# Performance work log

Measured on AMD Instinct MI355X. Metric: run time of the kernel, lower is better.

## Reference

```python
import jax, jax.numpy as jnp
import numpy as np
from jax import lax

NUM_CNNS = 300
INPUT_LEN = 608
NUM_CLASSES = 50
FILTER = 19
POOL = 7
HIDDEN = 100
BATCH = 256
L_CONV = INPUT_LEN - FILTER + 1          # 590
L_POOL = (L_CONV - POOL) // POOL + 1     # 84
EPS = 1e-5


def setup_inputs() -> dict:
    key = jax.random.key(0)
    ks = jax.random.split(key, 24)
    U, H = NUM_CNNS, HIDDEN
    d = {}
    d["x"] = jax.random.normal(ks[0], (BATCH, 4, INPUT_LEN), dtype=jnp.float32)
    # conv1: grouped Conv1d(4*U -> U, k=19, groups=U) on replicated input == dense Conv1d(4 -> U)
    d["w1"] = jax.random.normal(ks[1], (U, 4, FILTER), dtype=jnp.float32) * 0.1
    d["b1"] = jax.random.normal(ks[2], (U,), dtype=jnp.float32) * 0.05
    d["g1"] = jax.random.uniform(ks[3], (U,), dtype=jnp.float32, minval=0.5, maxval=1.5)
    d["be1"] = jax.random.normal(ks[4], (U,), dtype=jnp.float32) * 0.05
    d["m1"] = jax.random.normal(ks[5], (U,), dtype=jnp.float32) * 0.05
    d["v1"] = jax.random.uniform(ks[6], (U,), dtype=jnp.float32, minval=0.5, maxval=1.5)
    # grouped 1x1 conv: per-unit Linear 84 -> 100
    d["w2"] = jax.random.normal(ks[7], (U, H, L_POOL), dtype=jnp.float32) * (1.0 / np.sqrt(L_POOL))
    d["b2"] = jax.random.normal(ks[8], (U, H), dtype=jnp.float32) * 0.05
    d["g2"] = jax.random.uniform(ks[9], (U, H), dtype=jnp.float32, minval=0.5, maxval=1.5)
    d["be2"] = jax.random.normal(ks[10], (U, H), dtype=jnp.float32) * 0.05
    d["m2"] = jax.random.normal(ks[11], (U, H), dtype=jnp.float32) * 0.05
    d["v2"] = jax.random.uniform(ks[12], (U, H), dtype=jnp.float32, minval=0.5, maxval=1.5)
    # grouped 1x1 conv: per-unit Linear 100 -> 1
    d["w3"] = jax.random.normal(ks[13], (U, H), dtype=jnp.float32) * (1.0 / np.sqrt(H))
    d["b3"] = jax.random.normal(ks[14], (U,), dtype=jnp.float32) * 0.05
    d["g3"] = jax.random.uniform(ks[15], (U,), dtype=jnp.float32, minval=0.5, maxval=1.5)
    d["be3"] = jax.random.normal(ks[16], (U,), dtype=jnp.float32) * 0.05
    d["m3"] = jax.random.normal(ks[17], (U,), dtype=jnp.float32) * 0.05
    d["v3"] = jax.random.uniform(ks[18], (U,), dtype=jnp.float32, minval=0.5, maxval=1.5)
    # final Linear(U -> num_classes)
    d["wf"] = jax.random.normal(ks[19], (NUM_CLASSES, U), dtype=jnp.float32) * (1.0 / np.sqrt(U))
    d["bf"] = jax.random.normal(ks[20], (NUM_CLASSES,), dtype=jnp.float32) * 0.05
    return d


def _bn(y, g, be, m, v):
    return (y - m) * (g * lax.rsqrt(v + EPS)) + be


def reference(x, w1, b1, g1, be1, m1, v1, w2, b2, g2, be2, m2, v2,
              w3, b3, g3, be3, m3, v3, wf, bf):
    # conv1 (replicate + grouped conv == dense conv over 4 channels)
    y = lax.conv_general_dilated(x, w1, window_strides=(1,), padding='VALID',
                                 dimension_numbers=('NCH', 'OIH', 'NCH'))  # [B,U,590]
    y = y + b1[None, :, None]
    y = _bn(y, g1[None, :, None], be1[None, :, None], m1[None, :, None], v1[None, :, None])
    y = jnp.exp(y)  # ExpActivation
    # MaxPool1d(7,7): 590 -> 84 (uses first 588 positions)
    B = y.shape[0]
    y = y[:, :, :L_POOL * POOL].reshape(B, NUM_CNNS, L_POOL, POOL).max(axis=-1)  # [B,U,84]
    # per-unit MLP 84 -> 100 (grouped 1x1 conv) + BN + ReLU (dropout is eval-mode identity)
    h = jnp.einsum('buf,uof->buo', y, w2) + b2[None]  # [B,U,100]
    h = _bn(h, g2[None], be2[None], m2[None], v2[None])
    h = jax.nn.relu(h)
    # per-unit 100 -> 1 + BN + ReLU
    z = jnp.einsum('buo,uo->bu', h, w3) + b3[None]  # [B,U]
    z = _bn(z, g3[None], be3[None], m3[None], v3[None])
    z = jax.nn.relu(z)
    # final Linear
    return z @ wf.T + bf
```

## Files before the change

kernel.cpp:

```cpp
#include <hip/hip_runtime.h>
#include <hip/hip_bf16.h>

#define BATCH    256
#define NU       300
#define LIN      608
#define FILT     19
#define LPOOL    84
#define POOL     7
#define HID      100
#define NCLS     50
#define EPS      1e-5f
#define KP       96
#define NP       112
#define LDK      104
#define WROW     104
#define WBROWS   320
#define TCHUNK   112
#define MTN      19
#define BH       128
#define CSTR     116

typedef __attribute__((ext_vector_type(8))) short short8;
typedef __attribute__((ext_vector_type(4))) float float4v;
typedef __attribute__((ext_vector_type(4))) unsigned short us4;

#define LDS_WAIT() __asm__ __volatile__("s_waitcnt lgkmcnt(0)" ::: "memory")

__device__ __forceinline__ unsigned short f2bf(float f) {
    unsigned u = __float_as_uint(f);
    u += 0x7fffu + ((u >> 16) & 1u);
    return (unsigned short)(u >> 16);
}
__device__ __forceinline__ float bf2f(unsigned short h) {
    return __uint_as_float(((unsigned)h) << 16);
}

__global__ void k_prep(const float* __restrict__ w1, const float* __restrict__ x,
                       const float* __restrict__ b1, const float* __restrict__ g1,
                       const float* __restrict__ be1, const float* __restrict__ m1,
                       const float* __restrict__ v1,
                       unsigned short* __restrict__ Wbh,
                       unsigned short* __restrict__ Wbl,
                       unsigned int* __restrict__ xc,
                       float2* __restrict__ s1c1)
{
    const int idx = blockIdx.x * 256 + threadIdx.x;
    const int NW = WBROWS * WROW;
    if (idx < NW) {
        const int u = idx / WROW, kk = idx - u * WROW;
        float wv = 0.f;
        if (u < NU && kk < 96) {
            const int c = kk / 24, tap = kk - 24 * c;
            if (tap < FILT) wv = w1[(u * 4 + c) * FILT + tap];
        }
        const unsigned short hi = f2bf(wv);
        Wbh[idx] = hi;
        Wbl[idx] = f2bf(wv - bf2f(hi));
    }
    const int j = idx - NW;
    if (j >= 0 && j < BATCH * 4 * LIN) {
        const float xv = x[j];
        const unsigned short hi = f2bf(xv);
        const unsigned short lo = f2bf(xv - bf2f(hi));
        xc[j] = (unsigned)hi | ((unsigned)lo << 16);
    }
    const int j2 = j - BATCH * 4 * LIN;
    if (j2 >= 0 && j2 < MTN * 16) {
        float2 v = {0.f, 0.f};
        if (j2 < NU) {
            const float s = g1[j2] * rsqrtf(v1[j2] + EPS);
            v.x = s;
            v.y = (b1[j2] - m1[j2]) * s + be1[j2];
        }
        s1c1[j2] = v;
    }
}

__global__ __launch_bounds__(256, 3)
void k_conv7d(const unsigned short* __restrict__ Wbh,
              const unsigned short* __restrict__ Wbl,
              const unsigned int* __restrict__ xc,
              const float2* __restrict__ s1c1,
              unsigned short* __restrict__ ypool)
{
    __shared__ __align__(16) unsigned short Bh[TCHUNK * LDK];
    __shared__ __align__(16) float Cs[4][16 * CSTR];

    const int tid = threadIdx.x;
    const int b   = blockIdx.x;
    const int tc  = blockIdx.y;
    const int t0  = TCHUNK * tc;
    const int NT  = (tc == 5) ? 2 : 7;

    for (int i = tid; i < TCHUNK * 12; i += 256) {
        const int trow = i / 12;
        if (trow >= 16 * NT) continue;
        const int rem   = i - 12 * trow;
        const int c     = rem / 3;
        const int third = rem - 3 * c;
        const int kkb   = 24 * c + 8 * third;
        const int tt0   = t0 + trow + 8 * third;
        const unsigned int* src = xc + ((b * 4 + c) * LIN + tt0);

        unsigned int w[8];
        if (third < 2 && tt0 + 8 <= LIN) {
            const uint4 v0 = *(const uint4*)(src);
            const uint4 v1 = *(const uint4*)(src + 4);
            w[0] = v0.x; w[1] = v0.y; w[2] = v0.z; w[3] = v0.w;
            w[4] = v1.x; w[5] = v1.y; w[6] = v1.z; w[7] = v1.w;
        } else {
#pragma unroll
            for (int j = 0; j < 8; ++j) {
                const int tap = 8 * third + j;
                const int tt  = tt0 + j;
                unsigned int v = 0;
                if (tap < FILT && tt < LIN) v = src[j];
                w[j] = v;
            }
        }
        short8 hv;
#pragma unroll
        for (int j = 0; j < 8; ++j) hv[j] = (short)(w[j] & 0xffffu);
        *(short8*)(&Bh[trow * LDK + kkb]) = hv;
    }
    __syncthreads();

    const int lane = tid & 63;
    const int n    = lane & 15;
    const int quad = lane >> 4;
    const int wave = tid >> 6;
    float* Csw = Cs[wave];

    const int u_l = lane & 15;
    const int wq  = lane >> 4;
    const int pg0 = 16 * tc + 4 * wq;

    const int jend = 5 * wave + ((wave == 3) ? 4 : 5);
    for (int mt0 = 5 * wave; mt0 < jend; mt0 += 2) {
        const bool two = (mt0 + 1 < jend);

        short8 a0h[3], a0l[3], a1h[3], a1l[3];
        {
            const unsigned short* wrh = Wbh + (size_t)(mt0 * 16 + n) * WROW;
            const unsigned short* wrl = Wbl + (size_t)(mt0 * 16 + n) * WROW;
#pragma unroll
            for (int s = 0; s < 3; ++s) {
                a0h[s] = *(const short8*)(wrh + 32 * s + 8 * quad);
                a0l[s] = *(const short8*)(wrl + 32 * s + 8 * quad);
            }
            const int m1r = two ? (mt0 + 1) : mt0;
            const unsigned short* wrh1 = Wbh + (size_t)(m1r * 16 + n) * WROW;
            const unsigned short* wrl1 = Wbl + (size_t)(m1r * 16 + n) * WROW;
#pragma unroll
            for (int s = 0; s < 3; ++s) {
                a1h[s] = *(const short8*)(wrh1 + 32 * s + 8 * quad);
                a1l[s] = *(const short8*)(wrl1 + 32 * s + 8 * quad);
            }
        }

        float4v acc[2][7];
#pragma unroll
        for (int t2 = 0; t2 < 2; ++t2)
#pragma unroll
            for (int nt = 0; nt < 7; ++nt)
                acc[t2][nt] = (float4v){0.f, 0.f, 0.f, 0.f};

#pragma unroll
        for (int nt = 0; nt < 7; ++nt) {
            if (nt < NT) {
                short8 bhf[3];
#pragma unroll
                for (int s = 0; s < 3; ++s)
                    bhf[s] = *(const short8*)(&Bh[(16 * nt + n) * LDK + 32 * s + 8 * quad]);
#pragma unroll
                for (int s = 0; s < 3; ++s)
                    acc[0][nt] = __builtin_amdgcn_mfma_f32_16x16x32_bf16(
                        bhf[s], a0h[s], acc[0][nt], 0, 0, 0);
#pragma unroll
                for (int s = 0; s < 3; ++s)
                    acc[0][nt] = __builtin_amdgcn_mfma_f32_16x16x32_bf16(
                        bhf[s], a0l[s], acc[0][nt], 0, 0, 0);
                if (two) {
#pragma unroll
                    for (int s = 0; s < 3; ++s)
                        acc[1][nt] = __builtin_amdgcn_mfma_f32_16x16x32_bf16(
                            bhf[s], a1h[s], acc[1][nt], 0, 0, 0);
#pragma unroll
                    for (int s = 0; s < 3; ++s)
                        acc[1][nt] = __builtin_amdgcn_mfma_f32_16x16x32_bf16(
                            bhf[s], a1l[s], acc[1][nt], 0, 0, 0);
                }
            }
        }

#pragma unroll
        for (int t2 = 0; t2 < 2; ++t2) {
            if (t2 == 1 && !two) break;
            const int mt = mt0 + t2;

            LDS_WAIT();
#pragma unroll
            for (int nt = 0; nt < 7; ++nt) {
                if (nt < NT)
                    *(float4v*)(&Csw[n * CSTR + 16 * nt + 4 * quad]) = acc[t2][nt];
            }
            LDS_WAIT();

            float rv[28];
#pragma unroll
            for (int r7 = 0; r7 < 7; ++r7)
                *(float4v*)(&rv[4 * r7]) =
                    *(const float4v*)(&Csw[u_l * CSTR + 28 * wq + 4 * r7]);

            const int uglob = mt * 16 + u_l;
            const float2 sc = s1c1[uglob];
            us4 pk;
#pragma unroll
            for (int w4 = 0; w4 < 4; ++w4) {
                const int pg = pg0 + w4;
                unsigned short ov = 0;
                if (pg < LPOOL) {
                    float m0 = fmaxf(rv[7 * w4 + 0], rv[7 * w4 + 1]);
                    float m1 = fmaxf(rv[7 * w4 + 2], rv[7 * w4 + 3]);
                    float m2 = fmaxf(rv[7 * w4 + 4], rv[7 * w4 + 5]);
                    m0 = fmaxf(m0, rv[7 * w4 + 6]);
                    ov = f2bf(__expf(fmaf(fmaxf(fmaxf(m0, m1), m2), sc.x, sc.y)));
                }
                pk[w4] = ov;
            }
            if (uglob < NU)
                *(us4*)(&ypool[((size_t)b * NU + uglob) * KP + pg0]) = pk;
        }
    }
}

__global__ __launch_bounds__(256, 3)
void k_mlp(const unsigned short* __restrict__ ypool,
           const float* __restrict__ w2, const float* __restrict__ b2,
           const float* __restrict__ g2, const float* __restrict__ be2,
           const float* __restrict__ m2, const float* __restrict__ v2,
           const float* __restrict__ w3, const float* __restrict__ b3,
           const float* __restrict__ g3, const float* __restrict__ be3,
           const float* __restrict__ m3, const float* __restrict__ v3,
           float* __restrict__ zbuf)
{
    __shared__ __align__(16) unsigned short As[NP * LDK];
    __shared__ __align__(16) unsigned short Bs[BH * LDK];
    __shared__ __align__(16) float4 cs4[NP];

    const int tid = threadIdx.x;
    const int u   = blockIdx.x;
    const int b0  = blockIdx.y * BH;

    {
        const float* src = w2 + (size_t)u * HID * LPOOL;
        for (int c = tid; c < HID * (LPOOL / 4); c += 256) {
            const int o  = c / (LPOOL / 4);
            const int kc = (c % (LPOOL / 4)) * 4;
            const float4 v = *(const float4*)(src + o * LPOOL + kc);
            unsigned short* d = &As[o * LDK + kc];
            d[0] = f2bf(v.x); d[1] = f2bf(v.y); d[2] = f2bf(v.z); d[3] = f2bf(v.w);
        }
        for (int c = tid; c < HID * 6; c += 256) {
            const int o = c / 6, kc = LPOOL + (c % 6) * 2;
            *(unsigned*)(&As[o * LDK + kc]) = 0;
        }
        for (int c = tid; c < (NP - HID) * (KP / 2); c += 256) {
            const int o = HID + c / (KP / 2), kc = (c % (KP / 2)) * 2;
            *(unsigned*)(&As[o * LDK + kc]) = 0;
        }
    }
    {
        const unsigned short* ys = ypool + (size_t)u * KP;
        for (int c = tid; c < BH * (KP / 8); c += 256) {
            const int n  = c / (KP / 8);
            const int kc = (c % (KP / 8)) * 8;
            *(short8*)(&Bs[n * LDK + kc]) =
                *(const short8*)(ys + (size_t)(b0 + n) * NU * KP + kc);
        }
    }
    if (tid < NP) {
        float4 cv = {0.f, 0.f, 0.f, 0.f};
        if (tid < HID) {
            const int uo = u * HID + tid;
            const float s = g2[uo] * rsqrtf(v2[uo] + EPS);
            cv.x = s;
            cv.y = (b2[uo] - m2[uo]) * s + be2[uo];
            cv.z = w3[uo];
        }
        cs4[tid] = cv;
    }
    __syncthreads();

    const int lane = tid & 63;
    const int wave = tid >> 6;
    const int col  = lane & 15;
    const int quad = lane >> 4;

    short8 bf_[2][3];
#pragma unroll
    for (int j = 0; j < 2; ++j) {
        const int brow = 16 * (2 * wave + j) + col;
#pragma unroll
        for (int s = 0; s < 3; ++s)
            bf_[j][s] = *(const short8*)(&Bs[brow * LDK + 32 * s + 8 * quad]);
    }

    float zp0 = 0.f, zp1 = 0.f;
#pragma unroll
    for (int mt = 0; mt < 7; ++mt) {
        short8 af[3];
#pragma unroll
        for (int s = 0; s < 3; ++s)
            af[s] = *(const short8*)(&As[(16 * mt + col) * LDK + 32 * s + 8 * quad]);

        float4v a0 = {0.f, 0.f, 0.f, 0.f}, a1 = {0.f, 0.f, 0.f, 0.f};
#pragma unroll
        for (int s = 0; s < 3; ++s) {
            a0 = __builtin_amdgcn_mfma_f32_16x16x32_bf16(af[s], bf_[0][s], a0, 0, 0, 0);
            a1 = __builtin_amdgcn_mfma_f32_16x16x32_bf16(af[s], bf_[1][s], a1, 0, 0, 0);
        }
#pragma unroll
        for (int r = 0; r < 4; ++r) {
            const float4 cv = cs4[16 * mt + 4 * quad + r];
            zp0 = fmaf(fmaxf(fmaf(a0[r], cv.x, cv.y), 0.f), cv.z, zp0);
            zp1 = fmaf(fmaxf(fmaf(a1[r], cv.x, cv.y), 0.f), cv.z, zp1);
        }
    }

    zp0 += __shfl_xor(zp0, 16); zp0 += __shfl_xor(zp0, 32);
    zp1 += __shfl_xor(zp1, 16); zp1 += __shfl_xor(zp1, 32);

    if (quad == 0) {
        const float s3 = g3[u] * rsqrtf(v3[u] + EPS);
        const float c3 = (b3[u] - m3[u]) * s3 + be3[u];
        const int bA = b0 + 16 * (2 * wave + 0) + col;
        const int bB = b0 + 16 * (2 * wave + 1) + col;
        zbuf[(size_t)u * BATCH + bA] = fmaxf(fmaf(zp0, s3, c3), 0.f);
        zbuf[(size_t)u * BATCH + bB] = fmaxf(fmaf(zp1, s3, c3), 0.f);
    }
}

__global__ __launch_bounds__(256, 4)
void k_final(const float* __restrict__ zbuf, const float* __restrict__ wf,
             const float* __restrict__ bf, float* __restrict__ out)
{
    __shared__ float red[4][64];
    const int nc   = blockIdx.x;
    const int bq   = blockIdx.y;
    const int lane = threadIdx.x & 63;
    const int wave = threadIdx.x >> 6;
    const int b    = bq * 64 + lane;

    float a0 = 0.f, a1 = 0.f, a2 = 0.f;
    const int u0 = wave * 75;
#pragma unroll 5
    for (int i = 0; i < 75; i += 3) {
        a0 = fmaf(zbuf[(size_t)(u0 + i + 0) * BATCH + b], wf[nc * NU + u0 + i + 0], a0);
        a1 = fmaf(zbuf[(size_t)(u0 + i + 1) * BATCH + b], wf[nc * NU + u0 + i + 1], a1);
        a2 = fmaf(zbuf[(size_t)(u0 + i + 2) * BATCH + b], wf[nc * NU + u0 + i + 2], a2);
    }
    red[wave][lane] = (a0 + a1) + a2;
    __syncthreads();
    if (threadIdx.x < 64) {
        const float s = (red[0][lane] + red[1][lane]) + (red[2][lane] + red[3][lane]);
        out[(size_t)b * NCLS + nc] = s + bf[nc];
    }
}

extern "C" void kernel_launch(void* const* d_in, const int* in_sizes, int n_in,
                              void* d_out, int out_size, void* d_ws, size_t ws_size,
                              hipStream_t stream)
{
    const float* x   = (const float*)d_in[0];
    const float* w1  = (const float*)d_in[1];
    const float* b1  = (const float*)d_in[2];
    const float* g1  = (const float*)d_in[3];
    const float* be1 = (const float*)d_in[4];
    const float* m1  = (const float*)d_in[5];
    const float* v1  = (const float*)d_in[6];
    const float* w2  = (const float*)d_in[7];
    const float* b2  = (const float*)d_in[8];
    const float* g2  = (const float*)d_in[9];
    const float* be2 = (const float*)d_in[10];
    const float* m2  = (const float*)d_in[11];
    const float* v2  = (const float*)d_in[12];
    const float* w3  = (const float*)d_in[13];
    const float* b3  = (const float*)d_in[14];
    const float* g3  = (const float*)d_in[15];
    const float* be3 = (const float*)d_in[16];
    const float* m3  = (const float*)d_in[17];
    const float* v3  = (const float*)d_in[18];
    const float* wf  = (const float*)d_in[19];
    const float* bf  = (const float*)d_in[20];

    unsigned short* ypool = (unsigned short*)d_ws;
    float* zbuf = (float*)((char*)d_ws + 14745600);
    unsigned short* Wbh = (unsigned short*)((char*)d_ws + 15052800);
    unsigned short* Wbl = (unsigned short*)((char*)d_ws + 15119360);
    unsigned int*   xc  = (unsigned int*)((char*)d_ws + 15185920);
    float2*         sc1 = (float2*)((char*)d_ws + 17676288);

    const int prep_elems = WBROWS * WROW + BATCH * 4 * LIN + MTN * 16;
    k_prep<<<(prep_elems + 255) / 256, 256, 0, stream>>>(
        w1, x, b1, g1, be1, m1, v1, Wbh, Wbl, xc, sc1);

    dim3 gc(BATCH, 6);
    k_conv7d<<<gc, 256, 0, stream>>>(Wbh, Wbl, xc, sc1, ypool);

    dim3 gm(NU, BATCH / BH);
    k_mlp<<<gm, 256, 0, stream>>>(ypool, w2, b2, g2, be2, m2, v2,
                                  w3, b3, g3, be3, m3, v3, zbuf);

    dim3 gf(NCLS, 4);
    k_final<<<gf, 256, 0, stream>>>(zbuf, wf, bf, (float*)d_out);
}
```

Measured before the change: 149.1 us.

## Precompute padded bf16 w2 in prep and drop LDS staging in MLP kernel

The fp32-to-bf16 conversion and padding of the per-unit w2 weights moves out of k_mlp into the prep kernel, which writes a padded bf16 copy laid out for MFMA fragment loads. k_mlp no longer stages weights or activations in shared memory. Each wave loads its A and B fragments straight from global memory. The batch tile shrinks from 128 to 64, doubling the grid, and the occupancy hint rises to 4 blocks per SM. This removes the LDS fill, its barrier cost and the repeated fp32 conversion. In exchange it adds a prep pass over all of w2, scattered global fragment reads, and more re-reads of the weight copy across batch tiles.

```diff
diff --git a/kernel.cpp b/kernel.cpp
--- a/kernel.cpp
+++ b/kernel.cpp
@@ -17,7 +17,6 @@
 #define WBROWS   320
 #define TCHUNK   112
 #define MTN      19
-#define BH       128
 #define CSTR     116
 
 typedef __attribute__((ext_vector_type(8))) short short8;
@@ -38,11 +37,12 @@
 __global__ void k_prep(const float* __restrict__ w1, const float* __restrict__ x,
                        const float* __restrict__ b1, const float* __restrict__ g1,
                        const float* __restrict__ be1, const float* __restrict__ m1,
-                       const float* __restrict__ v1,
+                       const float* __restrict__ v1, const float* __restrict__ w2,
                        unsigned short* __restrict__ Wbh,
                        unsigned short* __restrict__ Wbl,
                        unsigned int* __restrict__ xc,
-                       float2* __restrict__ s1c1)
+                       float2* __restrict__ s1c1,
+                       unsigned short* __restrict__ w2c)
 {
     const int idx = blockIdx.x * 256 + threadIdx.x;
     const int NW = WBROWS * WROW;
@@ -73,6 +73,16 @@
             v.y = (b1[j2] - m1[j2]) * s + be1[j2];
         }
         s1c1[j2] = v;
+    }
+    const int j3 = j2 - MTN * 16;
+    if (j3 >= 0 && j3 < NU * NP * LDK) {
+        const int u  = j3 / (NP * LDK);
+        const int r  = j3 - u * (NP * LDK);
+        const int o  = r / LDK;
+        const int kc = r - o * LDK;
+        float wv = 0.f;
+        if (o < HID && kc < LPOOL) wv = w2[((size_t)u * HID + o) * LPOOL + kc];
+        w2c[j3] = f2bf(wv);
     }
 }
 
@@ -234,51 +244,23 @@
     }
 }
 
-__global__ __launch_bounds__(256, 3)
+__global__ __launch_bounds__(256, 4)
 void k_mlp(const unsigned short* __restrict__ ypool,
-           const float* __restrict__ w2, const float* __restrict__ b2,
-           const float* __restrict__ g2, const float* __restrict__ be2,
-           const float* __restrict__ m2, const float* __restrict__ v2,
+           const unsigned short* __restrict__ w2c,
+           const float* __restrict__ g2, const float* __restrict__ b2,
+           const float* __restrict__ be2, const float* __restrict__ m2,
+           const float* __restrict__ v2,
            const float* __restrict__ w3, const float* __restrict__ b3,
            const float* __restrict__ g3, const float* __restrict__ be3,
            const float* __restrict__ m3, const float* __restrict__ v3,
            float* __restrict__ zbuf)
 {
-    __shared__ __align__(16) unsigned short As[NP * LDK];
-    __shared__ __align__(16) unsigned short Bs[BH * LDK];
     __shared__ __align__(16) float4 cs4[NP];
 
     const int tid = threadIdx.x;
     const int u   = blockIdx.x;
-    const int b0  = blockIdx.y * BH;
-
-    {
-        const float* src = w2 + (size_t)u * HID * LPOOL;
-        for (int c = tid; c < HID * (LPOOL / 4); c += 256) {
-            const int o  = c / (LPOOL / 4);
-            const int kc = (c % (LPOOL / 4)) * 4;
-            const float4 v = *(const float4*)(src + o * LPOOL + kc);
-            unsigned short* d = &As[o * LDK + kc];
-            d[0] = f2bf(v.x); d[1] = f2bf(v.y); d[2] = f2bf(v.z); d[3] = f2bf(v.w);
-        }
-        for (int c = tid; c < HID * 6; c += 256) {
-            const int o = c / 6, kc = LPOOL + (c % 6) * 2;
-            *(unsigned*)(&As[o * LDK + kc]) = 0;
-        }
-        for (int c = tid; c < (NP - HID) * (KP / 2); c += 256) {
-            const int o = HID + c / (KP / 2), kc = (c % (KP / 2)) * 2;
-            *(unsigned*)(&As[o * LDK + kc]) = 0;
-        }
-    }
-    {
-        const unsigned short* ys = ypool + (size_t)u * KP;
-        for (int c = tid; c < BH * (KP / 8); c += 256) {
-            const int n  = c / (KP / 8);
-            const int kc = (c % (KP / 8)) * 8;
-            *(short8*)(&Bs[n * LDK + kc]) =
-                *(const short8*)(ys + (size_t)(b0 + n) * NU * KP + kc);
-        }
-    }
+    const int b0  = blockIdx.y * 64;
+
     if (tid < NP) {
         float4 cv = {0.f, 0.f, 0.f, 0.f};
         if (tid < HID) {
@@ -296,48 +278,43 @@
     const int wave = tid >> 6;
     const int col  = lane & 15;
     const int quad = lane >> 4;
-
-    short8 bf_[2][3];
-#pragma unroll
-    for (int j = 0; j < 2; ++j) {
-        const int brow = 16 * (2 * wave + j) + col;
+    const int bb   = b0 + 16 * wave + col;
+
+    short8 bf_[3];
+    {
+        const unsigned short* yrow = ypool + ((size_t)bb * NU + u) * KP;
 #pragma unroll
         for (int s = 0; s < 3; ++s)
-            bf_[j][s] = *(const short8*)(&Bs[brow * LDK + 32 * s + 8 * quad]);
-    }
-
-    float zp0 = 0.f, zp1 = 0.f;
+            bf_[s] = *(const short8*)(yrow + 32 * s + 8 * quad);
+    }
+
+    const unsigned short* wbase = w2c + (size_t)u * (NP * LDK);
+    float zp = 0.f;
 #pragma unroll
     for (int mt = 0; mt < 7; ++mt) {
         short8 af[3];
 #pragma unroll
         for (int s = 0; s < 3; ++s)
-            af[s] = *(const short8*)(&As[(16 * mt + col) * LDK + 32 * s + 8 * quad]);
-
-        float4v a0 = {0.f, 0.f, 0.f, 0.f}, a1 = {0.f, 0.f, 0.f, 0.f};
-#pragma unroll
-        for (int s = 0; s < 3; ++s) {
-            a0 = __builtin_amdgcn_mfma_f32_16x16x32_bf16(af[s], bf_[0][s], a0, 0, 0, 0);
-            a1 = __builtin_amdgcn_mfma_f32_16x16x32_bf16(af[s], bf_[1][s], a1, 0, 0, 0);
-        }
+            af[s] = *(const short8*)(wbase + (16 * mt + col) * LDK + 32 * s + 8 * quad);
+
+        float4v a0 = {0.f, 0.f, 0.f, 0.f};
+#pragma unroll
+        for (int s = 0; s < 3; ++s)
+            a0 = __builtin_amdgcn_mfma_f32_16x16x32_bf16(af[s], bf_[s], a0, 0, 0, 0);
 #pragma unroll
         for (int r = 0; r < 4; ++r) {
             const float4 cv = cs4[16 * mt + 4 * quad + r];
-            zp0 = fmaf(fmaxf(fmaf(a0[r], cv.x, cv.y), 0.f), cv.z, zp0);
-            zp1 = fmaf(fmaxf(fmaf(a1[r], cv.x, cv.y), 0.f), cv.z, zp1);
-        }
-    }
-
-    zp0 += __shfl_xor(zp0, 16); zp0 += __shfl_xor(zp0, 32);
-    zp1 += __shfl_xor(zp1, 16); zp1 += __shfl_xor(zp1, 32);
+            zp = fmaf(fmaxf(fmaf(a0[r], cv.x, cv.y), 0.f), cv.z, zp);
+        }
+    }
+
+    zp += __shfl_xor(zp, 16);
+    zp += __shfl_xor(zp, 32);
 
     if (quad == 0) {
         const float s3 = g3[u] * rsqrtf(v3[u] + EPS);
         const float c3 = (b3[u] - m3[u]) * s3 + be3[u];
-        const int bA = b0 + 16 * (2 * wave + 0) + col;
-        const int bB = b0 + 16 * (2 * wave + 1) + col;
-        zbuf[(size_t)u * BATCH + bA] = fmaxf(fmaf(zp0, s3, c3), 0.f);
-        zbuf[(size_t)u * BATCH + bB] = fmaxf(fmaf(zp1, s3, c3), 0.f);
+        zbuf[(size_t)u * BATCH + bb] = fmaxf(fmaf(zp, s3, c3), 0.f);
     }
 }
 
@@ -400,16 +377,17 @@
     unsigned short* Wbl = (unsigned short*)((char*)d_ws + 15119360);
     unsigned int*   xc  = (unsigned int*)((char*)d_ws + 15185920);
     float2*         sc1 = (float2*)((char*)d_ws + 17676288);
-
-    const int prep_elems = WBROWS * WROW + BATCH * 4 * LIN + MTN * 16;
+    unsigned short* w2c = (unsigned short*)((char*)d_ws + 17678720);
+
+    const int prep_elems = WBROWS * WROW + BATCH * 4 * LIN + MTN * 16 + NU * NP * LDK;
     k_prep<<<(prep_elems + 255) / 256, 256, 0, stream>>>(
-        w1, x, b1, g1, be1, m1, v1, Wbh, Wbl, xc, sc1);
+        w1, x, b1, g1, be1, m1, v1, w2, Wbh, Wbl, xc, sc1, w2c);
 
     dim3 gc(BATCH, 6);
     k_conv7d<<<gc, 256, 0, stream>>>(Wbh, Wbl, xc, sc1, ypool);
 
-    dim3 gm(NU, BATCH / BH);
-    k_mlp<<<gm, 256, 0, stream>>>(ypool, w2, b2, g2, be2, m2, v2,
+    dim3 gm(NU, BATCH / 64);
+    k_mlp<<<gm, 256, 0, stream>>>(ypool, w2c, g2, b2, be2, m2, v2,
                                   w3, b3, g3, be3, m3, v3, zbuf);
 
     dim3 gf(NCLS, 4);
```

Measured after the change: 150.7 us. No clear change (+1.0%).
